# Kernel tuning notes

Measured on AMD Instinct MI355X. Metric: run time of the kernel, lower is better.

The kernel has to match this reference:

```python
import jax, jax.numpy as jnp
import numpy as np

D_IN, D_H, D_OUT = 1024, 1024, 1024
D_MOE = 4096
N_EXPERTS = 8
TOP_K = 2


def setup_inputs() -> dict:
    key = jax.random.key(0)
    ks = jax.random.split(key, 10)
    s = lambda d: 1.0 / np.sqrt(d)
    x = jax.random.normal(ks[0], (2, 2048, D_IN), dtype=jnp.float32)
    W_in = jax.random.normal(ks[1], (D_IN, D_H), dtype=jnp.float32) * s(D_IN)
    b_in = jnp.zeros((D_H,), jnp.float32)
    W_gate = jax.random.normal(ks[2], (D_H, N_EXPERTS), dtype=jnp.float32) * s(D_H)
    b_gate = jnp.zeros((N_EXPERTS,), jnp.float32)
    W1 = jax.random.normal(ks[3], (N_EXPERTS, D_H, D_MOE), dtype=jnp.float32) * s(D_H)
    b1 = jnp.zeros((N_EXPERTS, D_MOE), jnp.float32)
    W2 = jax.random.normal(ks[4], (N_EXPERTS, D_MOE, D_H), dtype=jnp.float32) * s(D_MOE)
    b2 = jnp.zeros((N_EXPERTS, D_H), jnp.float32)
    W_out = jax.random.normal(ks[5], (D_H, D_OUT), dtype=jnp.float32) * s(D_H)
    b_out = jnp.zeros((D_OUT,), jnp.float32)
    return {"x": x, "W_in": W_in, "b_in": b_in, "W_gate": W_gate, "b_gate": b_gate,
            "W1": W1, "b1": b1, "W2": W2, "b2": b2, "W_out": W_out, "b_out": b_out}


def reference(x, W_in, b_in, W_gate, b_gate, W1, b1, W2, b2, W_out, b_out):
    B, S, _ = x.shape
    h = x @ W_in + b_in                       # [B,S,D_H]
    t = h.reshape(B * S, -1)                  # tokens [N,D_H]

    # --- top-k softmax gating ---
    logits = t @ W_gate + b_gate              # [N,E]
    probs = jax.nn.softmax(logits, axis=-1)
    topv, topi = jax.lax.top_k(probs, TOP_K)  # [N,k]
    topv = topv / jnp.sum(topv, axis=-1, keepdims=True)
    # dense routing weights [N,E] (zeros for unselected experts)
    route = jnp.zeros_like(probs).at[jnp.arange(t.shape[0])[:, None], topi].set(topv)

    # --- expert MLPs (dense all-expert compute, weighted combine) ---
    mid = jax.nn.relu(jnp.einsum('nd,edh->neh', t, W1) + b1)   # [N,E,D_MOE]
    eout = jnp.einsum('neh,ehd->ned', mid, W2) + b2            # [N,E,D_H]
    moe_out = jnp.einsum('ne,ned->nd', route, eout)            # [N,D_H]

    out = moe_out.reshape(B, S, -1) @ W_out + b_out            # [B,S,D_OUT]
    return out
```

## Files before the change

### kernel.cpp

```cpp
#include <hip/hip_runtime.h>
#include <hip/hip_bf16.h>

typedef __bf16 bf16_t;
typedef bf16_t bf16x8 __attribute__((ext_vector_type(8)));
typedef bf16_t bf16x4 __attribute__((ext_vector_type(4)));
typedef float f32x4 __attribute__((ext_vector_type(4)));

#define DIN 1024
#define DH 1024
#define DMOE 4096
#define NEXP 8
#define NTOK 4096

__device__ __forceinline__ void gload_lds16(const bf16_t* g, bf16_t* l) {
  __builtin_amdgcn_global_load_lds(
      (const __attribute__((address_space(1))) void*)g,
      (__attribute__((address_space(3))) void*)l, 16, 0, 0);
}

__device__ __forceinline__ void transpose_tile(const float* __restrict__ s,
                                               bf16_t* __restrict__ d, int R, int C,
                                               int tx, int ty, void* smem) {
  float (*tile)[65] = (float(*)[65])smem;
  const int c0 = tx * 64, r0 = ty * 64;
  const int t = threadIdx.x;
  const int rr = t >> 4;
  const int cc = (t & 15) << 2;
#pragma unroll
  for (int i = 0; i < 64; i += 16) {
    const float4 v = *(const float4*)&s[(size_t)(r0 + rr + i) * C + c0 + cc];
    tile[rr + i][cc + 0] = v.x;
    tile[rr + i][cc + 1] = v.y;
    tile[rr + i][cc + 2] = v.z;
    tile[rr + i][cc + 3] = v.w;
  }
  __syncthreads();
  const int orr = (t & 7) * 8;
  const int oc = t >> 3;
#pragma unroll
  for (int i = 0; i < 64; i += 32) {
    bf16x8 o;
#pragma unroll
    for (int j = 0; j < 8; ++j) o[j] = (bf16_t)tile[orr + j][oc + i];
    *(bf16x8*)&d[(size_t)(c0 + oc + i) * R + r0 + orr] = o;
  }
}

__global__ void k_prep_small(const float* __restrict__ W_in, const float* __restrict__ x,
                             const float* __restrict__ Wgate, const float* __restrict__ b_in,
                             const float* __restrict__ b_gate,
                             bf16_t* __restrict__ WtIn, bf16_t* __restrict__ xbf,
                             double* __restrict__ G, double* __restrict__ cvec,
                             int* __restrict__ cnt) {
  const int z = blockIdx.x;
  if (z < 256) {
    __shared__ float tile[64][65];
    transpose_tile(W_in, WtIn, DIN, DH, z & 15, z >> 4, tile);
    return;
  }
  if (z < 4352) {
    const int i = (z - 256) * 256 + threadIdx.x;
    const float4 v = *(const float4*)(x + (size_t)i * 4);
    bf16x4 o;
    o.x = (bf16_t)v.x; o.y = (bf16_t)v.y; o.z = (bf16_t)v.z; o.w = (bf16_t)v.w;
    *(bf16x4*)(xbf + (size_t)i * 4) = o;
    return;
  }
  const int b = z - 4352;
  if (b == 0 && threadIdx.x < 8) cnt[threadIdx.x] = 0;
  const int lane = threadIdx.x & 63;
  const int wave = b * 4 + (threadIdx.x >> 6);
  for (int d = wave; d <= DIN; d += 256) {
    const float* row = (d < DIN) ? (W_in + (size_t)d * DH) : b_in;
    double acc[8] = {0, 0, 0, 0, 0, 0, 0, 0};
    for (int k = lane; k < DH; k += 64) {
      const double xv = (double)row[k];
      const float* g = Wgate + (size_t)k * NEXP;
#pragma unroll
      for (int ee = 0; ee < 8; ++ee) acc[ee] += xv * (double)g[ee];
    }
#pragma unroll
    for (int ee = 0; ee < 8; ++ee) {
      double a = acc[ee];
      for (int o = 32; o > 0; o >>= 1) a += __shfl_down(a, o);
      acc[ee] = a;
    }
    if (lane == 0) {
      if (d < DIN) {
#pragma unroll
        for (int ee = 0; ee < 8; ++ee) G[(size_t)d * 8 + ee] = acc[ee];
      } else {
#pragma unroll
        for (int ee = 0; ee < 8; ++ee) cvec[ee] = acc[ee] + (double)b_gate[ee];
      }
    }
  }
}

__global__ void k_combine(const bf16_t* __restrict__ eout, bf16_t* __restrict__ moebf) {
  const int i = blockIdx.x * blockDim.x + threadIdx.x;
  const int t = i >> 8;
  const int q = (i & 255) * 4;
  const bf16x4 a = *(const bf16x4*)(eout + ((size_t)t * 2) * DH + q);
  const bf16x4 b = *(const bf16x4*)(eout + ((size_t)t * 2 + 1) * DH + q);
  bf16x4 o;
  o.x = (bf16_t)((float)a.x + (float)b.x);
  o.y = (bf16_t)((float)a.y + (float)b.y);
  o.z = (bf16_t)((float)a.z + (float)b.z);
  o.w = (bf16_t)((float)a.w + (float)b.w);
  *(bf16x4*)(moebf + (size_t)t * DH + q) = o;
}

__global__ __launch_bounds__(256, 3) void k_mega(
    const bf16_t* __restrict__ A, const bf16_t* __restrict__ B,
    const float* __restrict__ bias, bf16_t* __restrict__ Cbase,
    const float* __restrict__ x, const double* __restrict__ G,
    const double* __restrict__ cvec, int* __restrict__ cnt,
    int* __restrict__ list, float* __restrict__ wlist,
    const float* __restrict__ W1, const float* __restrict__ W2,
    const float* __restrict__ W_out,
    bf16_t* __restrict__ Wt1, bf16_t* __restrict__ Wt2, bf16_t* __restrict__ WtOut) {
  constexpr int N = DH, K = DIN;

  __shared__ bf16_t As[3][128 * 32];
  __shared__ bf16_t Bs[3][128 * 32];

  if (blockIdx.z >= 5) {
    const int t6 = (blockIdx.z - 5) * 256 + blockIdx.y * 8 + blockIdx.x;
    if (t6 < 8192) {
      const int e = t6 >> 10, tt = t6 & 1023;
      transpose_tile(W1 + (size_t)e * DH * DMOE, Wt1 + (size_t)e * DH * DMOE,
                     DH, DMOE, tt & 63, tt >> 6, As);
    } else if (t6 < 16384) {
      const int l = t6 - 8192, e = l >> 10, tt = l & 1023;
      transpose_tile(W2 + (size_t)e * DMOE * DH, Wt2 + (size_t)e * DMOE * DH,
                     DMOE, DH, tt & 15, tt >> 4, As);
    } else {
      const int tt = t6 - 16384;
      transpose_tile(W_out, WtOut, DH, DH, tt & 15, tt >> 4, As);
    }
    return;
  }

  if (blockIdx.z > 0) {
    const int lane = threadIdx.x & 63;
    const int bl = (blockIdx.z - 1) * 256 + blockIdx.y * 8 + blockIdx.x;
    const int t = bl * 4 + (threadIdx.x >> 6);
    const float* xr = x + (size_t)t * DIN;
    double acc[8] = {0, 0, 0, 0, 0, 0, 0, 0};
    for (int d = lane; d < DIN; d += 64) {
      const double xv = (double)xr[d];
      const double* g = G + (size_t)d * 8;
#pragma unroll
      for (int ee = 0; ee < 8; ++ee) acc[ee] += xv * g[ee];
    }
#pragma unroll
    for (int ee = 0; ee < 8; ++ee) {
      double a = acc[ee];
      for (int o = 32; o > 0; o >>= 1) a += __shfl_down(a, o);
      acc[ee] = a;
    }
    if (lane == 0) {
      double l[8];
#pragma unroll
      for (int ee = 0; ee < 8; ++ee) l[ee] = acc[ee] + cvec[ee];
      double m = l[0];
#pragma unroll
      for (int ee = 1; ee < 8; ++ee) m = fmax(m, l[ee]);
      double p[8];
#pragma unroll
      for (int ee = 0; ee < 8; ++ee) p[ee] = exp(l[ee] - m);
      int i1 = 0;
#pragma unroll
      for (int ee = 1; ee < 8; ++ee)
        if (p[ee] > p[i1]) i1 = ee;
      int i2 = (i1 == 0) ? 1 : 0;
#pragma unroll
      for (int ee = 0; ee < 8; ++ee)
        if (ee != i1 && p[ee] > p[i2]) i2 = ee;
      const double s2 = p[i1] + p[i2];
      const float w1 = (float)(p[i1] / s2);
      const float w2 = (float)(p[i2] / s2);
      int lp = atomicAdd(&cnt[i1], 1);
      list[i1 * NTOK + lp] = t * 2;
      wlist[i1 * NTOK + lp] = w1;
      lp = atomicAdd(&cnt[i2], 1);
      list[i2 * NTOK + lp] = t * 2 + 1;
      wlist[i2 * NTOK + lp] = w2;
    }
    return;
  }

  const int mblk = blockIdx.y, nblk = blockIdx.x;

  const int tid = threadIdx.x;
  const int lane = tid & 63;
  const int wid = tid >> 6;
  const int wr = wid >> 1, wc = wid & 1;

  const int srow0 = wid * 32 + (lane >> 2);
  const int srow1 = srow0 + 16;
  const int skcol = ((lane & 3) ^ ((lane >> 3) & 3)) * 8;

  const bf16_t* aptr0 = A + (size_t)(mblk * 128 + srow0) * K + skcol;
  const bf16_t* aptr1 = A + (size_t)(mblk * 128 + srow1) * K + skcol;
  const bf16_t* bptr0 = B + (size_t)(nblk * 128 + srow0) * K + skcol;
  const bf16_t* bptr1 = B + (size_t)(nblk * 128 + srow1) * K + skcol;

  const int ldsOfsA0 = (wid * 32) * 32;
  const int ldsOfsA1 = (wid * 32 + 16) * 32;

  f32x4 acc[4][4] = {};
  const int nkt = K >> 5;

  auto stage = [&](int buf, int kt) {
    const size_t ko = (size_t)kt * 32;
    gload_lds16(aptr0 + ko, &As[buf][ldsOfsA0]);
    gload_lds16(aptr1 + ko, &As[buf][ldsOfsA1]);
    gload_lds16(bptr0 + ko, &Bs[buf][ldsOfsA0]);
    gload_lds16(bptr1 + ko, &Bs[buf][ldsOfsA1]);
  };

  stage(0, 0);
  if (nkt > 1) stage(1, 1);

  const int fr = lane & 15;
  const int s0 = (((lane >> 4) ^ ((fr >> 1) & 3)) << 3);

  int cur = 0;
  for (int kt = 0; kt < nkt; ++kt) {
    int nxt = cur + 2;
    if (nxt >= 3) nxt -= 3;
    if (kt + 2 < nkt) {
      stage(nxt, kt + 2);
      asm volatile("s_waitcnt vmcnt(8)" ::: "memory");
    } else if (kt + 1 < nkt) {
      asm volatile("s_waitcnt vmcnt(4)" ::: "memory");
    } else {
      asm volatile("s_waitcnt vmcnt(0)" ::: "memory");
    }
    __builtin_amdgcn_s_barrier();

    bf16x8 af[4], bfr[4];
#pragma unroll
    for (int m = 0; m < 4; ++m)
      af[m] = *(const bf16x8*)&As[cur][(wr * 64 + m * 16 + fr) * 32 + s0];
#pragma unroll
    for (int n = 0; n < 4; ++n)
      bfr[n] = *(const bf16x8*)&Bs[cur][(wc * 64 + n * 16 + fr) * 32 + s0];
#pragma unroll
    for (int m = 0; m < 4; ++m)
#pragma unroll
      for (int n = 0; n < 4; ++n)
        acc[m][n] = __builtin_amdgcn_mfma_f32_16x16x32_bf16(af[m], bfr[n], acc[m][n], 0, 0, 0);

    __builtin_amdgcn_s_barrier();
    cur += 1;
    if (cur >= 3) cur -= 3;
  }

  const int colBase = nblk * 128 + wc * 64 + (lane & 15);
  const int rowBase = mblk * 128 + wr * 64 + ((lane >> 4) << 2);
#pragma unroll
  for (int n = 0; n < 4; ++n) {
    const int c = colBase + n * 16;
    const float bv = bias[c];
#pragma unroll
    for (int m = 0; m < 4; ++m) {
#pragma unroll
      for (int j = 0; j < 4; ++j) {
        const int r = rowBase + m * 16 + j;
        Cbase[(size_t)r * N + c] = (bf16_t)(acc[m][n][j] + bv);
      }
    }
  }
}

__global__ __launch_bounds__(256, 3) void k_gemm_out(
    const bf16_t* __restrict__ A, const bf16_t* __restrict__ B,
    const float* __restrict__ bias, float* __restrict__ Cbase,
    int M, int N, int K) {
  const int mblk = blockIdx.y, nblk = blockIdx.x;

  __shared__ bf16_t As[3][128 * 32];
  __shared__ bf16_t Bs[3][128 * 32];

  const int tid = threadIdx.x;
  const int lane = tid & 63;
  const int wid = tid >> 6;
  const int wr = wid >> 1, wc = wid & 1;

  const int srow0 = wid * 32 + (lane >> 2);
  const int srow1 = srow0 + 16;
  const int skcol = ((lane & 3) ^ ((lane >> 3) & 3)) * 8;

  const bf16_t* aptr0 = A + (size_t)(mblk * 128 + srow0) * K + skcol;
  const bf16_t* aptr1 = A + (size_t)(mblk * 128 + srow1) * K + skcol;
  const bf16_t* bptr0 = B + (size_t)(nblk * 128 + srow0) * K + skcol;
  const bf16_t* bptr1 = B + (size_t)(nblk * 128 + srow1) * K + skcol;

  const int ldsOfsA0 = (wid * 32) * 32;
  const int ldsOfsA1 = (wid * 32 + 16) * 32;

  f32x4 acc[4][4] = {};
  const int nkt = K >> 5;

  auto stage = [&](int buf, int kt) {
    const size_t ko = (size_t)kt * 32;
    gload_lds16(aptr0 + ko, &As[buf][ldsOfsA0]);
    gload_lds16(aptr1 + ko, &As[buf][ldsOfsA1]);
    gload_lds16(bptr0 + ko, &Bs[buf][ldsOfsA0]);
    gload_lds16(bptr1 + ko, &Bs[buf][ldsOfsA1]);
  };

  stage(0, 0);
  if (nkt > 1) stage(1, 1);

  const int fr = lane & 15;
  const int s0 = (((lane >> 4) ^ ((fr >> 1) & 3)) << 3);

  int cur = 0;
  for (int kt = 0; kt < nkt; ++kt) {
    int nxt = cur + 2;
    if (nxt >= 3) nxt -= 3;
    if (kt + 2 < nkt) {
      stage(nxt, kt + 2);
      asm volatile("s_waitcnt vmcnt(8)" ::: "memory");
    } else if (kt + 1 < nkt) {
      asm volatile("s_waitcnt vmcnt(4)" ::: "memory");
    } else {
      asm volatile("s_waitcnt vmcnt(0)" ::: "memory");
    }
    __builtin_amdgcn_s_barrier();

    bf16x8 af[4], bfr[4];
#pragma unroll
    for (int m = 0; m < 4; ++m)
      af[m] = *(const bf16x8*)&As[cur][(wr * 64 + m * 16 + fr) * 32 + s0];
#pragma unroll
    for (int n = 0; n < 4; ++n)
      bfr[n] = *(const bf16x8*)&Bs[cur][(wc * 64 + n * 16 + fr) * 32 + s0];
#pragma unroll
    for (int m = 0; m < 4; ++m)
#pragma unroll
      for (int n = 0; n < 4; ++n)
        acc[m][n] = __builtin_amdgcn_mfma_f32_16x16x32_bf16(af[m], bfr[n], acc[m][n], 0, 0, 0);

    __builtin_amdgcn_s_barrier();
    cur += 1;
    if (cur >= 3) cur -= 3;
  }

  const int colBase = nblk * 128 + wc * 64 + (lane & 15);
  const int rowBase = mblk * 128 + wr * 64 + ((lane >> 4) << 2);
#pragma unroll
  for (int n = 0; n < 4; ++n) {
    const int c = colBase + n * 16;
    const float bv = bias[c];
#pragma unroll
    for (int m = 0; m < 4; ++m) {
#pragma unroll
      for (int j = 0; j < 4; ++j) {
        const int r = rowBase + m * 16 + j;
        Cbase[(size_t)r * N + c] = acc[m][n][j] + bv;
      }
    }
  }
}

__global__ __launch_bounds__(512, 4) void k_gemm1(
    const bf16_t* __restrict__ Abase, const bf16_t* __restrict__ Bbase,
    const float* __restrict__ biasBase, bf16_t* __restrict__ Cbase,
    int N, int K,
    const int* __restrict__ cnt, const int* __restrict__ listBase) {
  const int e = blockIdx.z;
  const int mblk = blockIdx.y, nblk = blockIdx.x;
  const int Mloc = cnt[e];
  if (mblk * 256 >= Mloc) return;
  int rowOff = 0;
  for (int i = 0; i < NEXP; ++i) rowOff += (i < e) ? cnt[i] : 0;
  const bf16_t* B = Bbase + (size_t)e * N * K;
  const float* bias = biasBase + (size_t)e * N;
  const int* myList = listBase + e * NTOK;

  __shared__ bf16_t As[3][256 * 32];
  __shared__ bf16_t Bs[3][128 * 32];

  const int tid = threadIdx.x;
  const int lane = tid & 63;
  const int wid = tid >> 6;
  const int wr = wid >> 1, wc = wid & 1;

  const int subr = lane >> 2;
  const int skcol = ((lane & 3) ^ ((lane >> 3) & 3)) * 8;

  uint32_t aofs[2];
#pragma unroll
  for (int l = 0; l < 2; ++l) {
    int ar = mblk * 256 + (wid * 2 + l) * 16 + subr;
    if (ar > Mloc - 1) ar = Mloc - 1;
    aofs[l] = (uint32_t)(myList[ar] >> 1) * (uint32_t)K + skcol;
  }
  const uint32_t bofs = (uint32_t)(nblk * 128 + wid * 16 + subr) * (uint32_t)K + skcol;

  f32x4 acc[4][4] = {};
  const int nkt = K >> 5;

  auto stage = [&](int buf, int kt) {
    const uint32_t ko = (uint32_t)kt * 32;
    gload_lds16(Abase + aofs[0] + ko, &As[buf][(wid * 2 + 0) * 512]);
    gload_lds16(Abase + aofs[1] + ko, &As[buf][(wid * 2 + 1) * 512]);
    gload_lds16(B + bofs + ko, &Bs[buf][wid * 512]);
  };

  stage(0, 0);
  if (nkt > 1) stage(1, 1);

  const int fr = lane & 15;
  const int s0 = (((lane >> 4) ^ ((fr >> 1) & 3)) << 3);

  int cur = 0;
  for (int kt = 0; kt < nkt; ++kt) {
    int nxt = cur + 2;
    if (nxt >= 3) nxt -= 3;
    if (kt + 2 < nkt) {
      stage(nxt, kt + 2);
      asm volatile("s_waitcnt vmcnt(6)" ::: "memory");
    } else if (kt + 1 < nkt) {
      asm volatile("s_waitcnt vmcnt(3)" ::: "memory");
    } else {
      asm volatile("s_waitcnt vmcnt(0)" ::: "memory");
    }
    __builtin_amdgcn_s_barrier();

    bf16x8 af[4], bfr[4];
#pragma unroll
    for (int m = 0; m < 4; ++m)
      af[m] = *(const bf16x8*)&As[cur][(wr * 64 + m * 16 + fr) * 32 + s0];
#pragma unroll
    for (int n = 0; n < 4; ++n)
      bfr[n] = *(const bf16x8*)&Bs[cur][(wc * 64 + n * 16 + fr) * 32 + s0];
#pragma unroll
    for (int m = 0; m < 4; ++m)
#pragma unroll
      for (int n = 0; n < 4; ++n)
        acc[m][n] = __builtin_amdgcn_mfma_f32_16x16x32_bf16(af[m], bfr[n], acc[m][n], 0, 0, 0);

    __builtin_amdgcn_s_barrier();
    cur += 1;
    if (cur >= 3) cur -= 3;
  }

  const int colBase = nblk * 128 + wc * 64 + (lane & 15);
  const int rowBase = mblk * 256 + wr * 64 + ((lane >> 4) << 2);
#pragma unroll
  for (int n = 0; n < 4; ++n) {
    const int c = colBase + n * 16;
    const float bv = bias[c];
#pragma unroll
    for (int m = 0; m < 4; ++m) {
#pragma unroll
      for (int j = 0; j < 4; ++j) {
        const int r = rowBase + m * 16 + j;
        if (r < Mloc) {
          Cbase[(size_t)(rowOff + r) * N + c] = (bf16_t)fmaxf(acc[m][n][j] + bv, 0.0f);
        }
      }
    }
  }
}

__global__ __launch_bounds__(256, 3) void k_gemm_e2(
    const bf16_t* __restrict__ Abase, const bf16_t* __restrict__ Bbase,
    const float* __restrict__ biasBase, bf16_t* __restrict__ Cbase,
    int N, int K,
    const int* __restrict__ cnt, const int* __restrict__ listBase,
    const float* __restrict__ wlistBase) {
  const int e = blockIdx.z;
  const int mblk = blockIdx.y, nblk = blockIdx.x;
  const int Mloc = cnt[e];
  if (mblk * 128 >= Mloc) return;
  int rowOff = 0;
  for (int i = 0; i < NEXP; ++i) rowOff += (i < e) ? cnt[i] : 0;
  const bf16_t* B = Bbase + (size_t)e * N * K;
  const float* bias = biasBase + (size_t)e * N;
  const int* myList = listBase + e * NTOK;
  const float* myW = wlistBase + e * NTOK;
  const bf16_t* A = Abase + (size_t)rowOff * K;

  __shared__ bf16_t As[3][128 * 32];
  __shared__ bf16_t Bs[3][128 * 32];

  const int tid = threadIdx.x;
  const int lane = tid & 63;
  const int wid = tid >> 6;
  const int wr = wid >> 1, wc = wid & 1;

  const int srow0 = wid * 32 + (lane >> 2);
  const int srow1 = srow0 + 16;
  const int skcol = ((lane & 3) ^ ((lane >> 3) & 3)) * 8;

  int ar0 = mblk * 128 + srow0;
  int ar1 = mblk * 128 + srow1;
  if (ar0 > Mloc - 1) ar0 = Mloc - 1;
  if (ar1 > Mloc - 1) ar1 = Mloc - 1;
  const bf16_t* aptr0 = A + (size_t)ar0 * K + skcol;
  const bf16_t* aptr1 = A + (size_t)ar1 * K + skcol;
  const bf16_t* bptr0 = B + (size_t)(nblk * 128 + srow0) * K + skcol;
  const bf16_t* bptr1 = B + (size_t)(nblk * 128 + srow1) * K + skcol;

  const int ldsOfsA0 = (wid * 32) * 32;
  const int ldsOfsA1 = (wid * 32 + 16) * 32;

  f32x4 acc[4][4] = {};
  const int nkt = K >> 5;

  auto stage = [&](int buf, int kt) {
    const size_t ko = (size_t)kt * 32;
    gload_lds16(aptr0 + ko, &As[buf][ldsOfsA0]);
    gload_lds16(aptr1 + ko, &As[buf][ldsOfsA1]);
    gload_lds16(bptr0 + ko, &Bs[buf][ldsOfsA0]);
    gload_lds16(bptr1 + ko, &Bs[buf][ldsOfsA1]);
  };

  stage(0, 0);
  if (nkt > 1) stage(1, 1);

  const int fr = lane & 15;
  const int s0 = (((lane >> 4) ^ ((fr >> 1) & 3)) << 3);

  int cur = 0;
  for (int kt = 0; kt < nkt; ++kt) {
    int nxt = cur + 2;
    if (nxt >= 3) nxt -= 3;
    if (kt + 2 < nkt) {
      stage(nxt, kt + 2);
      asm volatile("s_waitcnt vmcnt(8)" ::: "memory");
    } else if (kt + 1 < nkt) {
      asm volatile("s_waitcnt vmcnt(4)" ::: "memory");
    } else {
      asm volatile("s_waitcnt vmcnt(0)" ::: "memory");
    }
    __builtin_amdgcn_s_barrier();

    bf16x8 af[4], bfr[4];
#pragma unroll
    for (int m = 0; m < 4; ++m)
      af[m] = *(const bf16x8*)&As[cur][(wr * 64 + m * 16 + fr) * 32 + s0];
#pragma unroll
    for (int n = 0; n < 4; ++n)
      bfr[n] = *(const bf16x8*)&Bs[cur][(wc * 64 + n * 16 + fr) * 32 + s0];
#pragma unroll
    for (int m = 0; m < 4; ++m)
#pragma unroll
      for (int n = 0; n < 4; ++n)
        acc[m][n] = __builtin_amdgcn_mfma_f32_16x16x32_bf16(af[m], bfr[n], acc[m][n], 0, 0, 0);

    __builtin_amdgcn_s_barrier();
    cur += 1;
    if (cur >= 3) cur -= 3;
  }

  const int colBase = nblk * 128 + wc * 64 + (lane & 15);
  const int rowBase = mblk * 128 + wr * 64 + ((lane >> 4) << 2);
#pragma unroll
  for (int n = 0; n < 4; ++n) {
    const int c = colBase + n * 16;
    const float bv = bias[c];
#pragma unroll
    for (int m = 0; m < 4; ++m) {
#pragma unroll
      for (int j = 0; j < 4; ++j) {
        const int r = rowBase + m * 16 + j;
        if (r < Mloc) {
          const int entry = myList[r];
          const float w = myW[r];
          Cbase[(size_t)entry * DH + c] = (bf16_t)((acc[m][n][j] + bv) * w);
        }
      }
    }
  }
}


extern "C" void kernel_launch(void* const* d_in, const int* in_sizes, int n_in,
                              void* d_out, int out_size, void* d_ws, size_t ws_size,
                              hipStream_t stream) {
  const float* x      = (const float*)d_in[0];
  const float* W_in   = (const float*)d_in[1];
  const float* b_in   = (const float*)d_in[2];
  const float* W_gate = (const float*)d_in[3];
  const float* b_gate = (const float*)d_in[4];
  const float* W1     = (const float*)d_in[5];
  const float* b1     = (const float*)d_in[6];
  const float* W2     = (const float*)d_in[7];
  const float* b2     = (const float*)d_in[8];
  const float* W_out  = (const float*)d_in[9];
  const float* b_out  = (const float*)d_in[10];

  char* ws = (char*)d_ws;
  size_t off = 0;
  auto alloc = [&](size_t bytes) -> void* {
    void* p = ws + off;
    off += (bytes + 255) & ~(size_t)255;
    return p;
  };

  bf16_t* WtIn  = (bf16_t*)alloc((size_t)DH * DIN * 2);
  bf16_t* Wt1   = (bf16_t*)alloc((size_t)NEXP * DMOE * DH * 2);
  bf16_t* Wt2   = (bf16_t*)alloc((size_t)NEXP * DH * DMOE * 2);
  bf16_t* WtOut = (bf16_t*)alloc((size_t)DH * DH * 2);
  bf16_t* xbf   = (bf16_t*)alloc((size_t)NTOK * DIN * 2);
  bf16_t* hbf   = (bf16_t*)alloc((size_t)NTOK * DH * 2);
  bf16_t* mid   = (bf16_t*)alloc((size_t)2 * NTOK * DMOE * 2);
  bf16_t* eoutb = (bf16_t*)alloc((size_t)2 * NTOK * DH * 2);
  bf16_t* moebf = (bf16_t*)alloc((size_t)NTOK * DH * 2);
  double* G     = (double*)alloc((size_t)DIN * 8 * 8);
  double* cvec  = (double*)alloc(8 * 8);
  int*    cnt   = (int*)alloc(NEXP * 4);
  int*    list  = (int*)alloc((size_t)NEXP * NTOK * 4);
  float*  wlist = (float*)alloc((size_t)NEXP * NTOK * 4);

  k_prep_small<<<4416, 256, 0, stream>>>(W_in, x, W_gate, b_in, b_gate,
                                         WtIn, xbf, G, cvec, cnt);

  k_mega<<<dim3(DH / 128, NTOK / 128, 70), 256, 0, stream>>>(
      xbf, WtIn, b_in, hbf, x, G, cvec, cnt, list, wlist,
      W1, W2, W_out, Wt1, Wt2, WtOut);

  k_gemm1<<<dim3(DMOE / 128, NTOK / 256, NEXP), 512, 0, stream>>>(
      hbf, Wt1, b1, mid, DMOE, DH, cnt, list);
  k_gemm_e2<<<dim3(DH / 128, NTOK / 128, NEXP), 256, 0, stream>>>(
      mid, Wt2, b2, eoutb, DH, DMOE, cnt, list, wlist);
  k_combine<<<NTOK * DH / 4 / 256, 256, 0, stream>>>(eoutb, moebf);
  k_gemm_out<<<dim3(DH / 128, NTOK / 128, 1), 256, 0, stream>>>(
      moebf, WtOut, b_out, (float*)d_out, NTOK, DH, DH);
}
```

Measured before the change: 514.5 us.

## Move W2 and W_out weight transposes into expert GEMM1 launch

Moves the fp32-to-bf16 transposes of W2 and W_out out of the first mega kernel and into extra z-slices of the expert GEMM1 launch, using a new 512-thread transpose helper. Only W1's transpose stays in k_mega, which now has fewer blocks, so its critical path is shorter. The moved transposes run alongside GEMM1 tiles and can overlap with them, filling idle CUs when expert counts are uneven. The cost is that GEMM1 tiles may compete for bandwidth, and the shared-memory declarations are hoisted to the top of the kernel.

```diff
diff --git a/kernel.cpp b/kernel.cpp
--- a/kernel.cpp
+++ b/kernel.cpp
@@ -44,6 +44,31 @@
     for (int j = 0; j < 8; ++j) o[j] = (bf16_t)tile[orr + j][oc + i];
     *(bf16x8*)&d[(size_t)(c0 + oc + i) * R + r0 + orr] = o;
   }
+}
+
+__device__ __forceinline__ void transpose_tile512(const float* __restrict__ s,
+                                                  bf16_t* __restrict__ d, int R, int C,
+                                                  int tx, int ty, void* smem) {
+  float (*tile)[65] = (float(*)[65])smem;
+  const int c0 = tx * 64, r0 = ty * 64;
+  const int t = threadIdx.x;
+  const int rr = t >> 4;
+  const int cc = (t & 15) << 2;
+#pragma unroll
+  for (int i = 0; i < 64; i += 32) {
+    const float4 v = *(const float4*)&s[(size_t)(r0 + rr + i) * C + c0 + cc];
+    tile[rr + i][cc + 0] = v.x;
+    tile[rr + i][cc + 1] = v.y;
+    tile[rr + i][cc + 2] = v.z;
+    tile[rr + i][cc + 3] = v.w;
+  }
+  __syncthreads();
+  const int orr = (t & 7) * 8;
+  const int oc = t >> 3;
+  bf16x8 o;
+#pragma unroll
+  for (int j = 0; j < 8; ++j) o[j] = (bf16_t)tile[orr + j][oc];
+  *(bf16x8*)&d[(size_t)(c0 + oc) * R + r0 + orr] = o;
 }
 
 __global__ void k_prep_small(const float* __restrict__ W_in, const float* __restrict__ x,
@@ -117,9 +142,7 @@
     const float* __restrict__ x, const double* __restrict__ G,
     const double* __restrict__ cvec, int* __restrict__ cnt,
     int* __restrict__ list, float* __restrict__ wlist,
-    const float* __restrict__ W1, const float* __restrict__ W2,
-    const float* __restrict__ W_out,
-    bf16_t* __restrict__ Wt1, bf16_t* __restrict__ Wt2, bf16_t* __restrict__ WtOut) {
+    const float* __restrict__ W1, bf16_t* __restrict__ Wt1) {
   constexpr int N = DH, K = DIN;
 
   __shared__ bf16_t As[3][128 * 32];
@@ -127,18 +150,9 @@
 
   if (blockIdx.z >= 5) {
     const int t6 = (blockIdx.z - 5) * 256 + blockIdx.y * 8 + blockIdx.x;
-    if (t6 < 8192) {
-      const int e = t6 >> 10, tt = t6 & 1023;
-      transpose_tile(W1 + (size_t)e * DH * DMOE, Wt1 + (size_t)e * DH * DMOE,
-                     DH, DMOE, tt & 63, tt >> 6, As);
-    } else if (t6 < 16384) {
-      const int l = t6 - 8192, e = l >> 10, tt = l & 1023;
-      transpose_tile(W2 + (size_t)e * DMOE * DH, Wt2 + (size_t)e * DMOE * DH,
-                     DMOE, DH, tt & 15, tt >> 4, As);
-    } else {
-      const int tt = t6 - 16384;
-      transpose_tile(W_out, WtOut, DH, DH, tt & 15, tt >> 4, As);
-    }
+    const int e = t6 >> 10, tt = t6 & 1023;
+    transpose_tile(W1 + (size_t)e * DH * DMOE, Wt1 + (size_t)e * DH * DMOE,
+                   DH, DMOE, tt & 63, tt >> 6, As);
     return;
   }
 
@@ -368,11 +382,29 @@
   }
 }
 
-__global__ __launch_bounds__(512, 4) void k_gemm1(
+__global__ __launch_bounds__(512, 4) void k_gemm1_t(
     const bf16_t* __restrict__ Abase, const bf16_t* __restrict__ Bbase,
     const float* __restrict__ biasBase, bf16_t* __restrict__ Cbase,
     int N, int K,
-    const int* __restrict__ cnt, const int* __restrict__ listBase) {
+    const int* __restrict__ cnt, const int* __restrict__ listBase,
+    const float* __restrict__ W2, const float* __restrict__ W_out,
+    bf16_t* __restrict__ Wt2, bf16_t* __restrict__ WtOut) {
+  __shared__ bf16_t As[3][256 * 32];
+  __shared__ bf16_t Bs[3][128 * 32];
+
+  if (blockIdx.z >= 8) {
+    const int t6 = (blockIdx.z - 8) * 512 + blockIdx.y * 32 + blockIdx.x;
+    if (t6 < 8192) {
+      const int e = t6 >> 10, tt = t6 & 1023;
+      transpose_tile512(W2 + (size_t)e * DMOE * DH, Wt2 + (size_t)e * DMOE * DH,
+                        DMOE, DH, tt & 15, tt >> 4, As);
+    } else if (t6 < 8448) {
+      const int tt = t6 - 8192;
+      transpose_tile512(W_out, WtOut, DH, DH, tt & 15, tt >> 4, As);
+    }
+    return;
+  }
+
   const int e = blockIdx.z;
   const int mblk = blockIdx.y, nblk = blockIdx.x;
   const int Mloc = cnt[e];
@@ -382,9 +414,6 @@
   const bf16_t* B = Bbase + (size_t)e * N * K;
   const float* bias = biasBase + (size_t)e * N;
   const int* myList = listBase + e * NTOK;
-
-  __shared__ bf16_t As[3][256 * 32];
-  __shared__ bf16_t Bs[3][128 * 32];
 
   const int tid = threadIdx.x;
   const int lane = tid & 63;
@@ -624,12 +653,12 @@
   k_prep_small<<<4416, 256, 0, stream>>>(W_in, x, W_gate, b_in, b_gate,
                                          WtIn, xbf, G, cvec, cnt);
 
-  k_mega<<<dim3(DH / 128, NTOK / 128, 70), 256, 0, stream>>>(
-      xbf, WtIn, b_in, hbf, x, G, cvec, cnt, list, wlist,
-      W1, W2, W_out, Wt1, Wt2, WtOut);
-
-  k_gemm1<<<dim3(DMOE / 128, NTOK / 256, NEXP), 512, 0, stream>>>(
-      hbf, Wt1, b1, mid, DMOE, DH, cnt, list);
+  k_mega<<<dim3(DH / 128, NTOK / 128, 37), 256, 0, stream>>>(
+      xbf, WtIn, b_in, hbf, x, G, cvec, cnt, list, wlist, W1, Wt1);
+
+  k_gemm1_t<<<dim3(DMOE / 128, NTOK / 256, 25), 512, 0, stream>>>(
+      hbf, Wt1, b1, mid, DMOE, DH, cnt, list, W2, W_out, Wt2, WtOut);
+
   k_gemm_e2<<<dim3(DH / 128, NTOK / 128, NEXP), 256, 0, stream>>>(
       mid, Wt2, b2, eoutb, DH, DMOE, cnt, list, wlist);
   k_combine<<<NTOK * DH / 4 / 256, 256, 0, stream>>>(eoutb, moebf);
```

New measurement: 490.4 us (median of 2 runs). 1.05x faster.
